# Kernel tuning notes

Measured on AMD Instinct MI355X. Metric: run time of the kernel, lower is better.

Reference implementation:

```python
import jax, jax.numpy as jnp
from jax import lax
import numpy as np

ALPHA = 0.5; EPS = 1e-6; RANK_PAIRS = 100
W_MEAN = 0.5; W_STD = 0.5
L_STAT = 1.0; L_RANK = 1.0; L_SMOOTH = 1.0
LABELS = np.array([5, 8, 13], dtype=np.int32)
TGT_CV = np.array([0.077, 0.227, 0.348], dtype=np.float32)


def _erode(mask_f):
    # torch: 1 - max_pool2d(1-x, k=3, pad=1); implicit -inf padding means
    # out-of-bounds pixels act as foreground -> min-pool with +inf init.
    return lax.reduce_window(mask_f, jnp.inf, lax.min, (3, 3), (1, 1), 'SAME') > 0.5


def _per_region(pred, pix, region, tgt_cv, key):
    # pred, pix: [H,W] float; region: [H,W] bool
    H, W = pred.shape
    HW = H * W
    regf = region.astype(jnp.float32)
    e1 = _erode(regf)
    e2 = _erode(e1.astype(jnp.float32))  # erode(region, iterations=2)
    core1 = jnp.where(jnp.sum(e1) < 2, region, e1)
    core2 = jnp.where(jnp.sum(e2) < 3, core1, e2)
    n_reg = jnp.sum(region)

    # ---- std (coefficient-of-variation) term on core2
    c2 = core2.astype(jnp.float32)
    n2 = jnp.sum(c2)
    n2s = jnp.maximum(n2, 1.0)
    mu = jnp.sum(pred * c2) / n2s
    var = jnp.sum(c2 * (pred - mu) ** 2) / n2s  # unbiased=False
    cv = jnp.sqrt(var) / (jnp.abs(mu) + EPS)
    std_val = jnp.abs(cv - tgt_cv)
    std_valid = (n_reg >= 3) & (n2 >= 3)

    # ---- pairwise rank term on core1 (sampled-pair path; realistic regions
    # always have n > full_pair_threshold=20)
    c1f = core1.reshape(-1).astype(jnp.float32)
    n1 = jnp.sum(c1f)
    p = jnp.where(n1 > 0, c1f / jnp.maximum(n1, 1.0), 1.0 / HW)
    k1, k2 = jax.random.split(key)
    ii = jax.random.choice(k1, HW, (RANK_PAIRS,), replace=True, p=p)
    jj = jax.random.choice(k2, HW, (RANK_PAIRS,), replace=True, p=p)
    pf = pred.reshape(-1)
    xf = pix.reshape(-1)
    s = jnp.sign(xf[ii] - xf[jj])
    pv = ((ii != jj) & (s != 0)).astype(jnp.float32)
    hinge = jax.nn.relu(-(pf[ii] - pf[jj]) * s)
    npv = jnp.sum(pv)
    rank_val = jnp.sum(hinge * pv) / jnp.maximum(npv, 1.0)
    rank_valid = (n_reg >= 2) & (n1 >= 2) & (npv > 0)

    # ---- smoothness term on core2
    dx = jnp.abs(pred[:, 1:] - pred[:, :-1])
    mx = (core2[:, 1:] & core2[:, :-1]).astype(jnp.float32)
    dy = jnp.abs(pred[1:, :] - pred[:-1, :])
    my = (core2[1:, :] & core2[:-1, :]).astype(jnp.float32)
    cx = jnp.sum(mx); cy = jnp.sum(my)
    mean_x = jnp.sum(dx * mx) / jnp.maximum(cx, 1.0)
    mean_y = jnp.sum(dy * my) / jnp.maximum(cy, 1.0)
    hx = (cx > 0).astype(jnp.float32); hy = (cy > 0).astype(jnp.float32)
    npres = hx + hy
    smooth_val = (mean_x * hx + mean_y * hy) / jnp.maximum(npres, 1.0)
    smooth_valid = (n_reg >= 3) & (n2 >= 3) & (npres > 0)

    return std_val, std_valid, rank_val, rank_valid, smooth_val, smooth_valid


def _masked_mean(v, valid):
    vf = valid.astype(jnp.float32)
    c = jnp.sum(vf)
    return jnp.where(c > 0, jnp.sum(v * vf) / jnp.maximum(c, 1.0), 0.0)


def _forward(pred, target, lab14, img1, img2):
    B, _, H, W = pred.shape
    p2 = pred[:, 0]
    lab = lab14[:, 0]
    t1 = img1[:, 0]
    t2 = img2[:, 0]
    pix = (1.0 - ALPHA) * (1.0 - t1) + ALPHA * t2  # pixel_map
    loss_mean = jnp.mean(jnp.abs(pred - target))

    labels = jnp.asarray(LABELS)
    regions = lab[:, None, :, :] == labels[None, :, None, None]  # [B,3,H,W]
    R = regions.reshape(B * 3, H, W)
    P = jnp.broadcast_to(p2[:, None], (B, 3, H, W)).reshape(B * 3, H, W)
    X = jnp.broadcast_to(pix[:, None], (B, 3, H, W)).reshape(B * 3, H, W)
    T = jnp.tile(jnp.asarray(TGT_CV), B)  # [B*3], label-minor matches reshape
    keys = jax.random.split(jax.random.key(42), B * 3)

    sv, svd, rv, rvd, mv, mvd = jax.vmap(_per_region)(P, X, R, T, keys)
    loss_std = _masked_mean(sv, svd)
    loss_rank = _masked_mean(rv, rvd)
    loss_smooth = _masked_mean(mv, mvd)

    loss_stat = W_MEAN * loss_mean + W_STD * loss_std
    return L_STAT * loss_stat + L_RANK * loss_rank + L_SMOOTH * loss_smooth


def setup_inputs() -> dict:
    key = jax.random.key(0)
    k1, k2, k3, k4, k5 = jax.random.split(key, 5)
    B, H, W = 16, 512, 512
    pred = jax.random.normal(k1, (B, 1, H, W), dtype=jnp.float32)
    target = jax.random.normal(k2, (B, 1, H, W), dtype=jnp.float32)
    lab14 = jax.random.randint(k3, (B, 1, H, W), 0, 15, dtype=jnp.int32)
    img1 = jax.random.uniform(k4, (B, 1, H, W), dtype=jnp.float32)
    img2 = jax.random.uniform(k5, (B, 1, H, W), dtype=jnp.float32)
    return {"pred": pred, "target": target, "lab14": lab14, "img1": img1, "img2": img2}


def reference(pred, target, lab14, img1, img2):
    return _forward(pred, target, lab14, img1, img2)
```

## Files before the change

kernel.cpp:

```cpp
#include <hip/hip_runtime.h>

#define BB 16
#define HH 512
#define WW 512
#define BH 8
#define NR (BH+5)
#define NBANDS (HH/BH)
#define NBLK (NBANDS*BB)
#define NREG 48
#define HWTOT (HH*WW)
#define MASK13 0x1FFFu

#define OFF_CNT48  0
#define OFF_SUM48  2048
#define OFF_RANKV  4608
#define OFF_RANKD  4800
#define OFF_CTR    5120
#define OFF_SUMSP  8192
#define OFF_CNTP   (OFF_SUMSP + NBLK*40*4)
#define OFF_MREG   (OFF_CNTP + NBLK*28*4)
#define MASKBYTES  (48LL*512*8*8)
#define OFF_ME1    (OFF_MREG + MASKBYTES)

__device__ __forceinline__ unsigned int hashu(unsigned int x) {
  x ^= x >> 16; x *= 0x7feb352dU; x ^= x >> 15; x *= 0x846ca68bU; x ^= x >> 16;
  return x;
}

__global__ __launch_bounds__(512, 4) void pass1_kernel(
    const float* __restrict__ pred, const float* __restrict__ target,
    const int* __restrict__ lab,
    float* __restrict__ sumsP, int* __restrict__ countsP,
    unsigned long long* __restrict__ mRegG, unsigned long long* __restrict__ mE1G,
    int* __restrict__ ctr)
{
  __shared__ unsigned long long XCH[514];
  __shared__ unsigned long long NB0[512];
  __shared__ unsigned int      NB2[512];
  __shared__ float RED[8][37];
  __shared__ unsigned int CNT[8][14];

  const int t    = threadIdx.x;
  const int lane = t & 63;
  const int wv   = t >> 6;
  const int c    = t;
  const int r0   = blockIdx.x * BH;
  const int b    = blockIdx.y;
  const int R    = r0 - 3;
  const int bandblk = b * NBANDS + blockIdx.x;

  if (blockIdx.x == 0 && b == 0 && t == 0) *ctr = 0;

  unsigned int OOR = 0;
  {
    int topClip = -R;
    if (topClip > 0) OOR |= (1u << topClip) - 1u;
    int botStart = HH - R;
    if (botStart < NR) OOR |= (~0u << botStart) & ((1u << NR) - 1u);
  }

  unsigned int colm0 = 0, colm1 = 0, colm2 = 0;
  #pragma unroll
  for (int lr = 0; lr < NR; ++lr) {
    int gy = R + lr;
    if ((unsigned)gy < (unsigned)HH) {
      int l = lab[((size_t)b*HH + gy)*WW + c];
      colm0 |= (l == 5)  ? (1u << lr) : 0u;
      colm1 |= (l == 8)  ? (1u << lr) : 0u;
      colm2 |= (l == 13) ? (1u << lr) : 0u;
    }
  }

  unsigned long long pk =  (unsigned long long)(colm0 | OOR)
        | ((unsigned long long)(colm1 | OOR) << 13)
        | ((unsigned long long)(colm2 | OOR) << 26);
  XCH[c+1] = pk;
  if (t == 0) { XCH[0] = ~0ull; XCH[513] = ~0ull; }
  __syncthreads();
  unsigned long long hp = pk & XCH[c] & XCH[c+2];
  unsigned int e1a[3];
  #pragma unroll
  for (int li = 0; li < 3; ++li) {
    unsigned int h = (unsigned int)((hp >> (13*li)) & MASK13);
    e1a[li] = h & (h >> 1) & (h << 1);
  }
  __syncthreads();
  unsigned long long pk2 =  (unsigned long long)((e1a[0] | OOR) & MASK13)
        | ((unsigned long long)((e1a[1] | OOR) & MASK13) << 13)
        | ((unsigned long long)((e1a[2] | OOR) & MASK13) << 26);
  XCH[c+1] = pk2;
  __syncthreads();
  unsigned long long hp2 = pk2 & XCH[c] & XCH[c+2];
  unsigned int e2a[3];
  #pragma unroll
  for (int li = 0; li < 3; ++li) {
    unsigned int h = (unsigned int)((hp2 >> (13*li)) & MASK13);
    e2a[li] = h & (h >> 1) & (h << 1);
  }

  unsigned int mS[9] = { colm0, e1a[0], e2a[0],
                         colm1, e1a[1], e2a[1],
                         colm2, e1a[2], e2a[2] };

  {
    unsigned long long p0 = 0;
    #pragma unroll
    for (int cb = 0; cb < 8; ++cb) p0 |= (unsigned long long)((mS[cb] >> 3) & 0xFFu) << (cb*8);
    NB0[c] = p0; NB2[c] = (mS[8] >> 3) & 0xFFu;
  }
  __syncthreads();
  unsigned long long nb0 = (c < 511) ? NB0[c+1] : 0ull;
  unsigned int       nb2 = (c < 511) ? NB2[c+1] : 0u;

  unsigned int W[9];
  const unsigned int nOOR = ~OOR;
  #pragma unroll
  for (int cb = 0; cb < 9; ++cb) {
    unsigned int w8  = (mS[cb] >> 3) & 0xFFu;
    unsigned int nbw = (cb < 8) ? ((unsigned int)(nb0 >> (cb*8)) & 0xFFu) : (nb2 & 0xFFu);
    unsigned int px8 = w8 & nbw;
    unsigned int mcl = mS[cb] & nOOR;
    unsigned int py8 = ((mcl & (mcl << 1)) >> 3) & 0xFFu;
    W[cb] = w8 | (px8 << 8) | (py8 << 16);
  }

  {
    unsigned long long myWord = 0;
    #pragma unroll
    for (int k = 0; k < 48; ++k) {
      const int ktype = k / 24, krem = k % 24, kli = krem >> 3, krow = krem & 7;
      unsigned int bit = (W[kli*3 + ktype] >> krow) & 1u;
      unsigned long long wrd = __ballot(bit != 0u);
      if (lane == k) myWord = wrd;
    }
    if (lane < 48) {
      int type = lane / 24, rem = lane % 24, li = rem >> 3, row = rem & 7;
      int gy = r0 + row;
      unsigned long long* dst = type ? mE1G : mRegG;
      dst[(((size_t)(b*3 + li))*HH + gy)*8 + wv] = myWord;
    }
  }

  {
    unsigned int pkc[14];
    #pragma unroll
    for (int j = 0; j < 14; ++j) pkc[j] = 0;
    #pragma unroll
    for (int cb = 0; cb < 9; ++cb) {
      unsigned int cnt = __popc(W[cb] & 0x0000FFu);
      unsigned int cx  = __popc(W[cb] & 0x00FF00u);
      unsigned int cy  = __popc(W[cb] & 0xFF0000u);
      int k0 = cb*3;
      pkc[(k0  )>>1] |= cnt << (((k0  )&1)*16);
      pkc[(k0+1)>>1] |= cx  << (((k0+1)&1)*16);
      pkc[(k0+2)>>1] |= cy  << (((k0+2)&1)*16);
    }
    #pragma unroll
    for (int j = 0; j < 14; ++j) {
      unsigned int v = pkc[j];
      for (int off = 32; off; off >>= 1) v += __shfl_down(v, off);
      if (lane == 0) CNT[wv][j] = v;
    }
  }

  float aP[9] = {}, aP2[9] = {}, aDX[9] = {}, aDY[9] = {};
  float aAbs = 0.f;
  const float* pB = pred   + (size_t)b*HH*WW;
  const float* tB = target + (size_t)b*HH*WW;
  float p_prev = (r0 > 0) ? pB[(size_t)(r0-1)*WW + c] : 0.f;
  const int cR = (c < 511) ? c + 1 : c;

  #pragma unroll
  for (int row = 0; row < BH; ++row) {
    const int gy = r0 + row;
    const float* prow = pB + (size_t)gy*WW;
    float p  = prow[c];
    float pr = prow[cR];
    float tg = tB[(size_t)gy*WW + c];
    aAbs += fabsf(p - tg);
    float d = fabsf(pr - p);
    float v = fabsf(p - p_prev);
    #pragma unroll
    for (int cb = 0; cb < 9; ++cb) {
      unsigned int c1 = (W[cb] >> row) & 1u;
      unsigned int px = (W[cb] >> (row + 8)) & 1u;
      unsigned int py = (W[cb] >> (row + 16)) & 1u;
      float f = c1 ? p : 0.f;
      aP[cb]  += f;
      aP2[cb]  = fmaf(f, p, aP2[cb]);
      aDX[cb] += px ? d : 0.f;
      aDY[cb] += py ? v : 0.f;
    }
    p_prev = p;
  }

  #pragma unroll
  for (int cb = 0; cb < 9; ++cb) {
    float s0 = aP[cb], s1 = aP2[cb], s2 = aDX[cb], s3 = aDY[cb];
    for (int off = 32; off; off >>= 1) {
      s0 += __shfl_down(s0, off);
      s1 += __shfl_down(s1, off);
      s2 += __shfl_down(s2, off);
      s3 += __shfl_down(s3, off);
    }
    if (lane == 0) {
      RED[wv][0*9 + cb] = s0; RED[wv][1*9 + cb] = s1;
      RED[wv][2*9 + cb] = s2; RED[wv][3*9 + cb] = s3;
    }
  }
  {
    float va = aAbs;
    for (int off = 32; off; off >>= 1) va += __shfl_down(va, off);
    if (lane == 0) RED[wv][36] = va;
  }
  __syncthreads();

  if (t < 37) {
    float s = 0.f;
    #pragma unroll
    for (int w = 0; w < 8; ++w) s += RED[w][t];
    sumsP[(size_t)bandblk*40 + t] = s;
  }
  if (t < 14) {
    unsigned int s = 0;
    #pragma unroll
    for (int w = 0; w < 8; ++w) s += CNT[w][t];
    countsP[bandblk*28 + 2*t]     = (int)(s & 0xFFFFu);
    countsP[bandblk*28 + 2*t + 1] = (int)(s >> 16);
  }
}

__global__ __launch_bounds__(256) void pass2_kernel(
    const float* __restrict__ pred, const float* __restrict__ img1,
    const float* __restrict__ img2,
    const unsigned long long* __restrict__ mRegG,
    const unsigned long long* __restrict__ mE1G,
    const float* __restrict__ sumsP, const int* __restrict__ countsP,
    int* __restrict__ counts48, float* __restrict__ sums48,
    float* __restrict__ rankval, int* __restrict__ rankvalid,
    int* __restrict__ ctr, float* __restrict__ out)
{
  const int r = blockIdx.x;
  const int b = r / 3, li = r % 3;
  const int t = threadIdx.x;
  const int lane = t & 63;
  const int wv   = t >> 6;
  __shared__ int LC[9];
  __shared__ int rowc[HH];
  __shared__ int pre[HH];
  __shared__ int grpPre[64];
  __shared__ int idxArr[200];
  __shared__ float redH[4];
  __shared__ int   redP[4];
  __shared__ int lastFlag;
  __shared__ double svvS[NREG], smvS[NREG];
  __shared__ int svdS[NREG], smdS[NREG];
  __shared__ double SAB[4];

  if (t < 9) LC[t] = 0;
  __syncthreads();
  for (int k = t; k < 9*NBANDS; k += 256) {
    int s9 = k >> 6, band = k & 63;
    int m = s9 / 3, st = s9 % 3;
    atomicAdd(&LC[s9], countsP[(b*NBANDS + band)*28 + (li*3 + m)*3 + st]);
  }
  if (wv == 0) {
    float sp[12];
    #pragma unroll
    for (int j = 0; j < 12; ++j) {
      int stat = j / 3, m = j % 3;
      sp[j] = sumsP[(size_t)(b*NBANDS + lane)*40 + stat*9 + li*3 + m];
    }
    #pragma unroll
    for (int j = 0; j < 12; ++j)
      for (int off = 32; off; off >>= 1) sp[j] += __shfl_down(sp[j], off);
    if (lane == 0) {
      #pragma unroll
      for (int j = 0; j < 12; ++j) atomicExch(&sums48[r*12 + j], sp[j]);
    }
  }
  __syncthreads();
  if (t < 9) atomicExch(&counts48[r*9 + t], LC[t]);

  int n_reg = LC[0], n_e1 = LC[3];
  int useE1 = (n_e1 >= 2);
  int n1 = useE1 ? n_e1 : n_reg;
  bool doRank = (n_reg >= 2 && n1 >= 2);
  float rv = 0.f; int rvd = 0;

  if (doRank) {
    const unsigned long long* M = (useE1 ? mE1G : mRegG) + (size_t)r*HH*8;
    {
      int row = t*2;
      int c0 = 0, c1v = 0;
      #pragma unroll
      for (int w = 0; w < 8; ++w) c0 += __popcll(M[(size_t)row*8 + w]);
      #pragma unroll
      for (int w = 0; w < 8; ++w) c1v += __popcll(M[(size_t)(row+1)*8 + w]);
      rowc[row] = c0; rowc[row+1] = c1v;
    }
    __syncthreads();
    if (t < 64) {
      int base = t*8, s = 0;
      #pragma unroll
      for (int k = 0; k < 8; ++k) s += rowc[base + k];
      int v = s;
      for (int off = 1; off < 64; off <<= 1) {
        int o = __shfl_up(v, off);
        if (t >= off) v += o;
      }
      grpPre[t] = v - s;
    }
    __syncthreads();
    if (t < 64) {
      int s = grpPre[t], base = t*8;
      #pragma unroll
      for (int k = 0; k < 8; ++k) { pre[base + k] = s; s += rowc[base + k]; }
    }
    __syncthreads();

    if (t < 200) {
      unsigned int h = hashu(0x9e3779b9u + (unsigned)(r*200 + t));
      float u = (float)(h >> 8) * (1.0f / 16777216.0f);
      int k = (int)(u * (float)n1);
      if (k >= n1) k = n1 - 1;
      if (k < 0) k = 0;
      int lo = 0, hi = HH;
      while (hi - lo > 1) { int mid = (lo + hi) >> 1; if (pre[mid] <= k) lo = mid; else hi = mid; }
      int row = lo;
      int local = k - pre[row];
      int idx = 0;
      #pragma unroll
      for (int w = 0; w < 8; ++w) {
        unsigned long long mm = M[(size_t)row*8 + w];
        int cc = __popcll(mm);
        if (local < cc) {
          for (int i = 0; i < local; ++i) mm &= mm - 1;
          idx = row*WW + w*64 + __builtin_ctzll(mm);
          local = 1 << 20;
        } else {
          local -= cc;
        }
      }
      idxArr[t] = idx;
    }
    __syncthreads();

    float hv = 0.f; int pv = 0;
    if (t < 100) {
      int ii = idxArr[t], jj = idxArr[t+100];
      size_t base = (size_t)b * HWTOT;
      float pi = pred[base+ii], pj = pred[base+jj];
      float xi = 0.5f*(1.f - img1[base+ii]) + 0.5f*img2[base+ii];
      float xj = 0.5f*(1.f - img1[base+jj]) + 0.5f*img2[base+jj];
      float s = (xi > xj) ? 1.f : ((xi < xj) ? -1.f : 0.f);
      pv = (ii != jj) && (s != 0.f);
      float hinge = fmaxf(0.f, -(pi - pj)*s);
      hv = pv ? hinge : 0.f;
    }
    for (int off = 32; off; off >>= 1) {
      hv += __shfl_down(hv, off);
      pv += __shfl_down(pv, off);
    }
    if (lane == 0) { redH[wv] = hv; redP[wv] = pv; }
    __syncthreads();
    if (t == 0) {
      float sh = redH[0] + redH[1] + redH[2] + redH[3];
      int   sp = redP[0] + redP[1] + redP[2] + redP[3];
      rv  = sh / (float)(sp > 0 ? sp : 1);
      rvd = (sp > 0) ? 1 : 0;
    }
  }

  __syncthreads();
  if (t == 0) {
    atomicExch(&rankval[r], rv);
    atomicExch(&rankvalid[r], rvd);
    __threadfence();
    int old = atomicAdd(ctr, 1);
    lastFlag = (old == NREG - 1);
  }
  __syncthreads();

  if (lastFlag) {
    __threadfence();
    double pa = 0.0;
    for (int k = t; k < NBLK; k += 256) pa += (double)sumsP[(size_t)k*40 + 36];
    for (int off = 32; off; off >>= 1) pa += __shfl_down(pa, off);
    if (lane == 0) SAB[wv] = pa;
    if (t < NREG) {
      const int* C = counts48 + t*9;
      const float* S = sums48 + t*12;
      int nr = C[0], ne1 = C[3], ne2 = C[6];
      int m1 = (ne1 < 2) ? 0 : 1;
      int m2 = (ne2 < 3) ? m1 : 2;
      int n2 = C[m2*3];
      double n2s = (double)(n2 > 1 ? n2 : 1);
      double mu  = (double)S[m2] / n2s;
      double var = (double)S[3+m2] / n2s - mu*mu;
      if (var < 0.0) var = 0.0;
      double cv = sqrt(var) / (fabs(mu) + 1e-6);
      int tli = t % 3;
      double tcv = (tli == 0) ? 0.077 : ((tli == 1) ? 0.227 : 0.348);
      svvS[t] = fabs(cv - tcv);
      svdS[t] = (nr >= 3 && n2 >= 3);
      int cx = C[m2*3+1], cy = C[m2*3+2];
      double mean_x = (double)S[6+m2] / (double)(cx > 1 ? cx : 1);
      double mean_y = (double)S[9+m2] / (double)(cy > 1 ? cy : 1);
      int hx = (cx > 0), hy = (cy > 0);
      int npres = hx + hy;
      smvS[t] = (mean_x*hx + mean_y*hy) / (double)(npres > 1 ? npres : 1);
      smdS[t] = (nr >= 3 && n2 >= 3 && npres > 0);
    }
    __syncthreads();
    if (t == 0) {
      double s_std = 0, s_sm = 0, s_rk = 0;
      int c_std = 0, c_sm = 0, c_rk = 0;
      for (int i = 0; i < NREG; ++i) {
        if (svdS[i])       { s_std += svvS[i];     c_std++; }
        if (smdS[i])       { s_sm  += smvS[i];     c_sm++;  }
        if (rankvalid[i])  { s_rk  += rankval[i];  c_rk++;  }
      }
      double loss_std = c_std ? s_std / c_std : 0.0;
      double loss_sm  = c_sm  ? s_sm  / c_sm  : 0.0;
      double loss_rk  = c_rk  ? s_rk  / c_rk  : 0.0;
      double loss_mean = (SAB[0] + SAB[1] + SAB[2] + SAB[3])
                         / (double)((long long)BB * HWTOT);
      out[0] = (float)(0.5*loss_mean + 0.5*loss_std + loss_rk + loss_sm);
    }
  }
}

extern "C" void kernel_launch(void* const* d_in, const int* in_sizes, int n_in,
                              void* d_out, int out_size, void* d_ws, size_t ws_size,
                              hipStream_t stream) {
  const float* pred   = (const float*)d_in[0];
  const float* target = (const float*)d_in[1];
  const int*   lab    = (const int*)d_in[2];
  const float* img1   = (const float*)d_in[3];
  const float* img2   = (const float*)d_in[4];
  float* out = (float*)d_out;
  char* ws = (char*)d_ws;

  int*    counts48 = (int*)(ws + OFF_CNT48);
  float*  sums48   = (float*)(ws + OFF_SUM48);
  float*  rankval  = (float*)(ws + OFF_RANKV);
  int*    rankvld  = (int*)(ws + OFF_RANKD);
  int*    ctr      = (int*)(ws + OFF_CTR);
  float*  sumsP    = (float*)(ws + OFF_SUMSP);
  int*    countsP  = (int*)(ws + OFF_CNTP);
  unsigned long long* mReg = (unsigned long long*)(ws + OFF_MREG);
  unsigned long long* mE1  = (unsigned long long*)(ws + OFF_ME1);

  dim3 g1(NBANDS, BB);
  pass1_kernel<<<g1, 512, 0, stream>>>(pred, target, lab, sumsP, countsP,
                                       mReg, mE1, ctr);
  pass2_kernel<<<NREG, 256, 0, stream>>>(pred, img1, img2, mReg, mE1,
                                         sumsP, countsP, counts48, sums48,
                                         rankval, rankvld, ctr, out);
}
```

Baseline: 167.7 us.

## Double pass1 band height and precompute per-row mask popcounts for pass2

```diff
diff --git a/kernel.cpp b/kernel.cpp
--- a/kernel.cpp
+++ b/kernel.cpp
@@ -3,13 +3,13 @@
 #define BB 16
 #define HH 512
 #define WW 512
-#define BH 8
+#define BH 16
 #define NR (BH+5)
 #define NBANDS (HH/BH)
 #define NBLK (NBANDS*BB)
 #define NREG 48
 #define HWTOT (HH*WW)
-#define MASK13 0x1FFFu
+#define MASK21 0x1FFFFFu
 
 #define OFF_CNT48  0
 #define OFF_SUM48  2048
@@ -18,7 +18,9 @@
 #define OFF_CTR    5120
 #define OFF_SUMSP  8192
 #define OFF_CNTP   (OFF_SUMSP + NBLK*40*4)
-#define OFF_MREG   (OFF_CNTP + NBLK*28*4)
+#define OFF_ROWCR  (OFF_CNTP + NBLK*28*4)
+#define OFF_ROWCE  (OFF_ROWCR + 48*512*4)
+#define OFF_MREG   (OFF_ROWCE + 48*512*4)
 #define MASKBYTES  (48LL*512*8*8)
 #define OFF_ME1    (OFF_MREG + MASKBYTES)
 
@@ -32,11 +34,14 @@
     const int* __restrict__ lab,
     float* __restrict__ sumsP, int* __restrict__ countsP,
     unsigned long long* __restrict__ mRegG, unsigned long long* __restrict__ mE1G,
+    int* __restrict__ rowcR, int* __restrict__ rowcE,
     int* __restrict__ ctr)
 {
   __shared__ unsigned long long XCH[514];
   __shared__ unsigned long long NB0[512];
+  __shared__ unsigned long long NB1[512];
   __shared__ unsigned int      NB2[512];
+  __shared__ int   RC[96];
   __shared__ float RED[8][37];
   __shared__ unsigned int CNT[8][14];
 
@@ -50,6 +55,7 @@
   const int bandblk = b * NBANDS + blockIdx.x;
 
   if (blockIdx.x == 0 && b == 0 && t == 0) *ctr = 0;
+  if (t < 96) RC[t] = 0;
 
   unsigned int OOR = 0;
   {
@@ -60,7 +66,6 @@
   }
 
   unsigned int colm0 = 0, colm1 = 0, colm2 = 0;
-  #pragma unroll
   for (int lr = 0; lr < NR; ++lr) {
     int gy = R + lr;
     if ((unsigned)gy < (unsigned)HH) {
@@ -72,8 +77,8 @@
   }
 
   unsigned long long pk =  (unsigned long long)(colm0 | OOR)
-        | ((unsigned long long)(colm1 | OOR) << 13)
-        | ((unsigned long long)(colm2 | OOR) << 26);
+        | ((unsigned long long)(colm1 | OOR) << 21)
+        | ((unsigned long long)(colm2 | OOR) << 42);
   XCH[c+1] = pk;
   if (t == 0) { XCH[0] = ~0ull; XCH[513] = ~0ull; }
   __syncthreads();
@@ -81,20 +86,20 @@
   unsigned int e1a[3];
   #pragma unroll
   for (int li = 0; li < 3; ++li) {
-    unsigned int h = (unsigned int)((hp >> (13*li)) & MASK13);
+    unsigned int h = (unsigned int)((hp >> (21*li)) & MASK21);
     e1a[li] = h & (h >> 1) & (h << 1);
   }
   __syncthreads();
-  unsigned long long pk2 =  (unsigned long long)((e1a[0] | OOR) & MASK13)
-        | ((unsigned long long)((e1a[1] | OOR) & MASK13) << 13)
-        | ((unsigned long long)((e1a[2] | OOR) & MASK13) << 26);
+  unsigned long long pk2 =  (unsigned long long)((e1a[0] | OOR) & MASK21)
+        | ((unsigned long long)((e1a[1] | OOR) & MASK21) << 21)
+        | ((unsigned long long)((e1a[2] | OOR) & MASK21) << 42);
   XCH[c+1] = pk2;
   __syncthreads();
   unsigned long long hp2 = pk2 & XCH[c] & XCH[c+2];
   unsigned int e2a[3];
   #pragma unroll
   for (int li = 0; li < 3; ++li) {
-    unsigned int h = (unsigned int)((hp2 >> (13*li)) & MASK13);
+    unsigned int h = (unsigned int)((hp2 >> (21*li)) & MASK21);
     e2a[li] = h & (h >> 1) & (h << 1);
   }
 
@@ -103,41 +108,55 @@
                          colm2, e1a[2], e2a[2] };
 
   {
-    unsigned long long p0 = 0;
-    #pragma unroll
-    for (int cb = 0; cb < 8; ++cb) p0 |= (unsigned long long)((mS[cb] >> 3) & 0xFFu) << (cb*8);
-    NB0[c] = p0; NB2[c] = (mS[8] >> 3) & 0xFFu;
+    unsigned long long p0 = 0, p1 = 0;
+    #pragma unroll
+    for (int cb = 0; cb < 4; ++cb) p0 |= (unsigned long long)((mS[cb] >> 3) & 0xFFFFu) << (cb*16);
+    #pragma unroll
+    for (int cb = 4; cb < 8; ++cb) p1 |= (unsigned long long)((mS[cb] >> 3) & 0xFFFFu) << ((cb-4)*16);
+    NB0[c] = p0; NB1[c] = p1; NB2[c] = (mS[8] >> 3) & 0xFFFFu;
   }
   __syncthreads();
   unsigned long long nb0 = (c < 511) ? NB0[c+1] : 0ull;
+  unsigned long long nb1 = (c < 511) ? NB1[c+1] : 0ull;
   unsigned int       nb2 = (c < 511) ? NB2[c+1] : 0u;
 
-  unsigned int W[9];
+  unsigned int W[9], Y[9];
   const unsigned int nOOR = ~OOR;
   #pragma unroll
   for (int cb = 0; cb < 9; ++cb) {
-    unsigned int w8  = (mS[cb] >> 3) & 0xFFu;
-    unsigned int nbw = (cb < 8) ? ((unsigned int)(nb0 >> (cb*8)) & 0xFFu) : (nb2 & 0xFFu);
-    unsigned int px8 = w8 & nbw;
+    unsigned int w16 = (mS[cb] >> 3) & 0xFFFFu;
+    unsigned int nbw;
+    if (cb < 4)      nbw = (unsigned int)(nb0 >> (cb*16)) & 0xFFFFu;
+    else if (cb < 8) nbw = (unsigned int)(nb1 >> ((cb-4)*16)) & 0xFFFFu;
+    else             nbw = nb2 & 0xFFFFu;
     unsigned int mcl = mS[cb] & nOOR;
-    unsigned int py8 = ((mcl & (mcl << 1)) >> 3) & 0xFFu;
-    W[cb] = w8 | (px8 << 8) | (py8 << 16);
-  }
-
-  {
-    unsigned long long myWord = 0;
-    #pragma unroll
-    for (int k = 0; k < 48; ++k) {
-      const int ktype = k / 24, krem = k % 24, kli = krem >> 3, krow = krem & 7;
+    unsigned int py16 = ((mcl & (mcl << 1)) >> 3) & 0xFFFFu;
+    W[cb] = w16 | ((w16 & nbw) << 16);
+    Y[cb] = py16;
+  }
+
+  {
+    unsigned long long w1 = 0, w2 = 0;
+    #pragma unroll
+    for (int k = 0; k < 96; ++k) {
+      const int ktype = k / 48, krem = k % 48, kli = krem >> 4, krow = krem & 15;
       unsigned int bit = (W[kli*3 + ktype] >> krow) & 1u;
       unsigned long long wrd = __ballot(bit != 0u);
-      if (lane == k) myWord = wrd;
-    }
-    if (lane < 48) {
-      int type = lane / 24, rem = lane % 24, li = rem >> 3, row = rem & 7;
-      int gy = r0 + row;
+      if (k < 64) { if (lane == k) w1 = wrd; }
+      else        { if (lane == (k-64)) w2 = wrd; }
+    }
+    {
+      int k = lane;
+      int type = k / 48, rem = k % 48, li = rem >> 4, row = rem & 15;
       unsigned long long* dst = type ? mE1G : mRegG;
-      dst[(((size_t)(b*3 + li))*HH + gy)*8 + wv] = myWord;
+      dst[(((size_t)(b*3 + li))*HH + (r0 + row))*8 + wv] = w1;
+      atomicAdd(&RC[k], (int)__popcll(w1));
+    }
+    if (lane < 32) {
+      int k = 64 + lane;
+      int rem = k % 48, li = rem >> 4, row = rem & 15;
+      mE1G[(((size_t)(b*3 + li))*HH + (r0 + row))*8 + wv] = w2;
+      atomicAdd(&RC[k], (int)__popcll(w2));
     }
   }
 
@@ -147,9 +166,9 @@
     for (int j = 0; j < 14; ++j) pkc[j] = 0;
     #pragma unroll
     for (int cb = 0; cb < 9; ++cb) {
-      unsigned int cnt = __popc(W[cb] & 0x0000FFu);
-      unsigned int cx  = __popc(W[cb] & 0x00FF00u);
-      unsigned int cy  = __popc(W[cb] & 0xFF0000u);
+      unsigned int cnt = __popc(W[cb] & 0xFFFFu);
+      unsigned int cx  = __popc(W[cb] >> 16);
+      unsigned int cy  = __popc(Y[cb]);
       int k0 = cb*3;
       pkc[(k0  )>>1] |= cnt << (((k0  )&1)*16);
       pkc[(k0+1)>>1] |= cx  << (((k0+1)&1)*16);
@@ -170,7 +189,6 @@
   float p_prev = (r0 > 0) ? pB[(size_t)(r0-1)*WW + c] : 0.f;
   const int cR = (c < 511) ? c + 1 : c;
 
-  #pragma unroll
   for (int row = 0; row < BH; ++row) {
     const int gy = r0 + row;
     const float* prow = pB + (size_t)gy*WW;
@@ -183,8 +201,8 @@
     #pragma unroll
     for (int cb = 0; cb < 9; ++cb) {
       unsigned int c1 = (W[cb] >> row) & 1u;
-      unsigned int px = (W[cb] >> (row + 8)) & 1u;
-      unsigned int py = (W[cb] >> (row + 16)) & 1u;
+      unsigned int px = (W[cb] >> (row + 16)) & 1u;
+      unsigned int py = (Y[cb] >> row) & 1u;
       float f = c1 ? p : 0.f;
       aP[cb]  += f;
       aP2[cb]  = fmaf(f, p, aP2[cb]);
@@ -228,6 +246,11 @@
     countsP[bandblk*28 + 2*t]     = (int)(s & 0xFFFFu);
     countsP[bandblk*28 + 2*t + 1] = (int)(s >> 16);
   }
+  if (t < 96) {
+    int type = t / 48, rem = t % 48, li = rem >> 4, row = rem & 15;
+    int* dst = type ? rowcE : rowcR;
+    dst[((size_t)(b*3 + li))*HH + (r0 + row)] = RC[t];
+  }
 }
 
 __global__ __launch_bounds__(256) void pass2_kernel(
@@ -236,6 +259,7 @@
     const unsigned long long* __restrict__ mRegG,
     const unsigned long long* __restrict__ mE1G,
     const float* __restrict__ sumsP, const int* __restrict__ countsP,
+    const int* __restrict__ rowcR, const int* __restrict__ rowcE,
     int* __restrict__ counts48, float* __restrict__ sums48,
     float* __restrict__ rankval, int* __restrict__ rankvalid,
     int* __restrict__ ctr, float* __restrict__ out)
@@ -246,9 +270,10 @@
   const int lane = t & 63;
   const int wv   = t >> 6;
   __shared__ int LC[9];
-  __shared__ int rowc[HH];
+  __shared__ int rcR[HH], rcE[HH];
   __shared__ int pre[HH];
   __shared__ int grpPre[64];
+  __shared__ int wsumR[4], wsumE[4];
   __shared__ int idxArr[200];
   __shared__ float redH[4];
   __shared__ int   redP[4];
@@ -258,18 +283,34 @@
   __shared__ double SAB[4];
 
   if (t < 9) LC[t] = 0;
-  __syncthreads();
+
+  int2 vR = ((const int2*)(rowcR + (size_t)r*HH))[t];
+  int2 vE = ((const int2*)(rowcE + (size_t)r*HH))[t];
+  rcR[2*t] = vR.x; rcR[2*t+1] = vR.y;
+  rcE[2*t] = vE.x; rcE[2*t+1] = vE.y;
+  {
+    int sR = vR.x + vR.y, sE = vE.x + vE.y;
+    for (int off = 32; off; off >>= 1) {
+      sR += __shfl_down(sR, off);
+      sE += __shfl_down(sE, off);
+    }
+    if (lane == 0) { wsumR[wv] = sR; wsumE[wv] = sE; }
+  }
+  __syncthreads();
+  int n_reg = wsumR[0] + wsumR[1] + wsumR[2] + wsumR[3];
+  int n_e1  = wsumE[0] + wsumE[1] + wsumE[2] + wsumE[3];
+
   for (int k = t; k < 9*NBANDS; k += 256) {
-    int s9 = k >> 6, band = k & 63;
-    int m = s9 / 3, st = s9 % 3;
-    atomicAdd(&LC[s9], countsP[(b*NBANDS + band)*28 + (li*3 + m)*3 + st]);
+    int s9 = k >> 5, band = k & 31;
+    atomicAdd(&LC[s9], countsP[(b*NBANDS + band)*28 + (li*3 + (s9/3))*3 + (s9%3)]);
   }
   if (wv == 0) {
     float sp[12];
     #pragma unroll
     for (int j = 0; j < 12; ++j) {
       int stat = j / 3, m = j % 3;
-      sp[j] = sumsP[(size_t)(b*NBANDS + lane)*40 + stat*9 + li*3 + m];
+      sp[j] = (lane < NBANDS)
+            ? sumsP[(size_t)(b*NBANDS + lane)*40 + stat*9 + li*3 + m] : 0.f;
     }
     #pragma unroll
     for (int j = 0; j < 12; ++j)
@@ -282,28 +323,17 @@
   __syncthreads();
   if (t < 9) atomicExch(&counts48[r*9 + t], LC[t]);
 
-  int n_reg = LC[0], n_e1 = LC[3];
   int useE1 = (n_e1 >= 2);
   int n1 = useE1 ? n_e1 : n_reg;
   bool doRank = (n_reg >= 2 && n1 >= 2);
   float rv = 0.f; int rvd = 0;
 
   if (doRank) {
-    const unsigned long long* M = (useE1 ? mE1G : mRegG) + (size_t)r*HH*8;
-    {
-      int row = t*2;
-      int c0 = 0, c1v = 0;
-      #pragma unroll
-      for (int w = 0; w < 8; ++w) c0 += __popcll(M[(size_t)row*8 + w]);
-      #pragma unroll
-      for (int w = 0; w < 8; ++w) c1v += __popcll(M[(size_t)(row+1)*8 + w]);
-      rowc[row] = c0; rowc[row+1] = c1v;
-    }
-    __syncthreads();
+    const int* rc = useE1 ? rcE : rcR;
     if (t < 64) {
       int base = t*8, s = 0;
       #pragma unroll
-      for (int k = 0; k < 8; ++k) s += rowc[base + k];
+      for (int k = 0; k < 8; ++k) s += rc[base + k];
       int v = s;
       for (int off = 1; off < 64; off <<= 1) {
         int o = __shfl_up(v, off);
@@ -315,10 +345,11 @@
     if (t < 64) {
       int s = grpPre[t], base = t*8;
       #pragma unroll
-      for (int k = 0; k < 8; ++k) { pre[base + k] = s; s += rowc[base + k]; }
+      for (int k = 0; k < 8; ++k) { pre[base + k] = s; s += rc[base + k]; }
     }
     __syncthreads();
 
+    const unsigned long long* M = (useE1 ? mE1G : mRegG) + (size_t)r*HH*8;
     if (t < 200) {
       unsigned int h = hashu(0x9e3779b9u + (unsigned)(r*200 + t));
       float u = (float)(h >> 8) * (1.0f / 16777216.0f);
@@ -449,13 +480,16 @@
   int*    ctr      = (int*)(ws + OFF_CTR);
   float*  sumsP    = (float*)(ws + OFF_SUMSP);
   int*    countsP  = (int*)(ws + OFF_CNTP);
+  int*    rowcR    = (int*)(ws + OFF_ROWCR);
+  int*    rowcE    = (int*)(ws + OFF_ROWCE);
   unsigned long long* mReg = (unsigned long long*)(ws + OFF_MREG);
   unsigned long long* mE1  = (unsigned long long*)(ws + OFF_ME1);
 
   dim3 g1(NBANDS, BB);
   pass1_kernel<<<g1, 512, 0, stream>>>(pred, target, lab, sumsP, countsP,
-                                       mReg, mE1, ctr);
+                                       mReg, mE1, rowcR, rowcE, ctr);
   pass2_kernel<<<NREG, 256, 0, stream>>>(pred, img1, img2, mReg, mE1,
-                                         sumsP, countsP, counts48, sums48,
+                                         sumsP, countsP, rowcR, rowcE,
+                                         counts48, sums48,
                                          rankval, rankvld, ctr, out);
 }
```

Measured after the change: 169.0 us. Within noise of the previous version (+0.8%).

## Accumulate stats only for core2 masks and compute fallbacks lazily in pass2

Applied to the files above, without the earlier changes.

```diff
diff --git a/kernel.cpp b/kernel.cpp
--- a/kernel.cpp
+++ b/kernel.cpp
@@ -11,16 +11,20 @@
 #define HWTOT (HH*WW)
 #define MASK13 0x1FFFu
 
-#define OFF_CNT48  0
-#define OFF_SUM48  2048
-#define OFF_RANKV  4608
-#define OFF_RANKD  4800
-#define OFF_CTR    5120
-#define OFF_SUMSP  8192
-#define OFF_CNTP   (OFF_SUMSP + NBLK*40*4)
-#define OFF_MREG   (OFF_CNTP + NBLK*28*4)
-#define MASKBYTES  (48LL*512*8*8)
-#define OFF_ME1    (OFF_MREG + MASKBYTES)
+#define OFF_SVV   0
+#define OFF_SVD   192
+#define OFF_SMV   384
+#define OFF_SMD   576
+#define OFF_RANKV 768
+#define OFF_RANKD 960
+#define OFF_CTR   1152
+#define OFF_SUMSP 4096
+#define OFF_CNTP  (OFF_SUMSP + NBLK*16*4)
+#define OFF_ROWCR (OFF_CNTP + NBLK*16*4)
+#define OFF_ROWCE (OFF_ROWCR + 48*512*4)
+#define OFF_MREG  (OFF_ROWCE + 48*512*4)
+#define MASKBYTES (48LL*512*8*8)
+#define OFF_ME1   (OFF_MREG + MASKBYTES)
 
 __device__ __forceinline__ unsigned int hashu(unsigned int x) {
   x ^= x >> 16; x *= 0x7feb352dU; x ^= x >> 15; x *= 0x846ca68bU; x ^= x >> 16;
@@ -32,13 +36,14 @@
     const int* __restrict__ lab,
     float* __restrict__ sumsP, int* __restrict__ countsP,
     unsigned long long* __restrict__ mRegG, unsigned long long* __restrict__ mE1G,
+    int* __restrict__ rowcR, int* __restrict__ rowcE,
     int* __restrict__ ctr)
 {
   __shared__ unsigned long long XCH[514];
-  __shared__ unsigned long long NB0[512];
-  __shared__ unsigned int      NB2[512];
-  __shared__ float RED[8][37];
-  __shared__ unsigned int CNT[8][14];
+  __shared__ unsigned int NBX[512];
+  __shared__ int   RC[48];
+  __shared__ float RED[8][13];
+  __shared__ unsigned int CNT[8][8];
 
   const int t    = threadIdx.x;
   const int lane = t & 63;
@@ -47,9 +52,10 @@
   const int r0   = blockIdx.x * BH;
   const int b    = blockIdx.y;
   const int R    = r0 - 3;
-  const int bandblk = b * NBANDS + blockIdx.x;
+  const int blk  = b * NBANDS + blockIdx.x;
 
   if (blockIdx.x == 0 && b == 0 && t == 0) *ctr = 0;
+  if (t < 48) RC[t] = 0;
 
   unsigned int OOR = 0;
   {
@@ -102,68 +108,62 @@
                          colm1, e1a[1], e2a[1],
                          colm2, e1a[2], e2a[2] };
 
-  {
-    unsigned long long p0 = 0;
-    #pragma unroll
-    for (int cb = 0; cb < 8; ++cb) p0 |= (unsigned long long)((mS[cb] >> 3) & 0xFFu) << (cb*8);
-    NB0[c] = p0; NB2[c] = (mS[8] >> 3) & 0xFFu;
-  }
-  __syncthreads();
-  unsigned long long nb0 = (c < 511) ? NB0[c+1] : 0ull;
-  unsigned int       nb2 = (c < 511) ? NB2[c+1] : 0u;
-
-  unsigned int W[9];
+  NBX[c] =  ((e2a[0] >> 3) & 0xFFu)
+         | (((e2a[1] >> 3) & 0xFFu) << 8)
+         | (((e2a[2] >> 3) & 0xFFu) << 16);
+  __syncthreads();
+  unsigned int nbx = (c < 511) ? NBX[c+1] : 0u;
+
+  unsigned int W2[3];
   const unsigned int nOOR = ~OOR;
   #pragma unroll
-  for (int cb = 0; cb < 9; ++cb) {
-    unsigned int w8  = (mS[cb] >> 3) & 0xFFu;
-    unsigned int nbw = (cb < 8) ? ((unsigned int)(nb0 >> (cb*8)) & 0xFFu) : (nb2 & 0xFFu);
-    unsigned int px8 = w8 & nbw;
-    unsigned int mcl = mS[cb] & nOOR;
+  for (int li = 0; li < 3; ++li) {
+    unsigned int w8  = (e2a[li] >> 3) & 0xFFu;
+    unsigned int nbw = (nbx >> (8*li)) & 0xFFu;
+    unsigned int mcl = e2a[li] & nOOR;
     unsigned int py8 = ((mcl & (mcl << 1)) >> 3) & 0xFFu;
-    W[cb] = w8 | (px8 << 8) | (py8 << 16);
+    W2[li] = w8 | ((w8 & nbw) << 8) | (py8 << 16);
   }
 
   {
-    unsigned long long myWord = 0;
+    unsigned long long w1 = 0;
     #pragma unroll
     for (int k = 0; k < 48; ++k) {
       const int ktype = k / 24, krem = k % 24, kli = krem >> 3, krow = krem & 7;
-      unsigned int bit = (W[kli*3 + ktype] >> krow) & 1u;
+      unsigned int bit = (mS[kli*3 + ktype] >> (krow + 3)) & 1u;
       unsigned long long wrd = __ballot(bit != 0u);
-      if (lane == k) myWord = wrd;
+      if (lane == k) w1 = wrd;
     }
     if (lane < 48) {
       int type = lane / 24, rem = lane % 24, li = rem >> 3, row = rem & 7;
-      int gy = r0 + row;
       unsigned long long* dst = type ? mE1G : mRegG;
-      dst[(((size_t)(b*3 + li))*HH + gy)*8 + wv] = myWord;
+      dst[(((size_t)(b*3 + li))*HH + (r0 + row))*8 + wv] = w1;
+      atomicAdd(&RC[lane], (int)__popcll(w1));
     }
   }
 
   {
-    unsigned int pkc[14];
-    #pragma unroll
-    for (int j = 0; j < 14; ++j) pkc[j] = 0;
-    #pragma unroll
-    for (int cb = 0; cb < 9; ++cb) {
-      unsigned int cnt = __popc(W[cb] & 0x0000FFu);
-      unsigned int cx  = __popc(W[cb] & 0x00FF00u);
-      unsigned int cy  = __popc(W[cb] & 0xFF0000u);
-      int k0 = cb*3;
-      pkc[(k0  )>>1] |= cnt << (((k0  )&1)*16);
-      pkc[(k0+1)>>1] |= cx  << (((k0+1)&1)*16);
-      pkc[(k0+2)>>1] |= cy  << (((k0+2)&1)*16);
-    }
-    #pragma unroll
-    for (int j = 0; j < 14; ++j) {
+    unsigned int v15[15];
+    #pragma unroll
+    for (int cb = 0; cb < 9; ++cb) v15[cb] = __popc((mS[cb] >> 3) & 0xFFu);
+    #pragma unroll
+    for (int li = 0; li < 3; ++li) {
+      v15[9+li]  = __popc(W2[li] & 0x00FF00u);
+      v15[12+li] = __popc(W2[li] & 0xFF0000u);
+    }
+    unsigned int pkc[8];
+    #pragma unroll
+    for (int j = 0; j < 7; ++j) pkc[j] = v15[2*j] | (v15[2*j+1] << 16);
+    pkc[7] = v15[14];
+    #pragma unroll
+    for (int j = 0; j < 8; ++j) {
       unsigned int v = pkc[j];
       for (int off = 32; off; off >>= 1) v += __shfl_down(v, off);
       if (lane == 0) CNT[wv][j] = v;
     }
   }
 
-  float aP[9] = {}, aP2[9] = {}, aDX[9] = {}, aDY[9] = {};
+  float aP[3] = {}, aP2[3] = {}, aDX[3] = {}, aDY[3] = {};
   float aAbs = 0.f;
   const float* pB = pred   + (size_t)b*HH*WW;
   const float* tB = target + (size_t)b*HH*WW;
@@ -181,52 +181,49 @@
     float d = fabsf(pr - p);
     float v = fabsf(p - p_prev);
     #pragma unroll
-    for (int cb = 0; cb < 9; ++cb) {
-      unsigned int c1 = (W[cb] >> row) & 1u;
-      unsigned int px = (W[cb] >> (row + 8)) & 1u;
-      unsigned int py = (W[cb] >> (row + 16)) & 1u;
+    for (int li = 0; li < 3; ++li) {
+      unsigned int c1 = (W2[li] >> row) & 1u;
+      unsigned int px = (W2[li] >> (row + 8)) & 1u;
+      unsigned int py = (W2[li] >> (row + 16)) & 1u;
       float f = c1 ? p : 0.f;
-      aP[cb]  += f;
-      aP2[cb]  = fmaf(f, p, aP2[cb]);
-      aDX[cb] += px ? d : 0.f;
-      aDY[cb] += py ? v : 0.f;
+      aP[li]  += f;
+      aP2[li]  = fmaf(f, p, aP2[li]);
+      aDX[li] += px ? d : 0.f;
+      aDY[li] += py ? v : 0.f;
     }
     p_prev = p;
   }
 
-  #pragma unroll
-  for (int cb = 0; cb < 9; ++cb) {
-    float s0 = aP[cb], s1 = aP2[cb], s2 = aDX[cb], s3 = aDY[cb];
-    for (int off = 32; off; off >>= 1) {
-      s0 += __shfl_down(s0, off);
-      s1 += __shfl_down(s1, off);
-      s2 += __shfl_down(s2, off);
-      s3 += __shfl_down(s3, off);
-    }
-    if (lane == 0) {
-      RED[wv][0*9 + cb] = s0; RED[wv][1*9 + cb] = s1;
-      RED[wv][2*9 + cb] = s2; RED[wv][3*9 + cb] = s3;
-    }
-  }
   {
-    float va = aAbs;
-    for (int off = 32; off; off >>= 1) va += __shfl_down(va, off);
-    if (lane == 0) RED[wv][36] = va;
-  }
-  __syncthreads();
-
-  if (t < 37) {
+    float a13[13] = { aP[0], aP2[0], aDX[0], aDY[0],
+                      aP[1], aP2[1], aDX[1], aDY[1],
+                      aP[2], aP2[2], aDX[2], aDY[2], aAbs };
+    #pragma unroll
+    for (int j = 0; j < 13; ++j) {
+      float s = a13[j];
+      for (int off = 32; off; off >>= 1) s += __shfl_down(s, off);
+      if (lane == 0) RED[wv][j] = s;
+    }
+  }
+  __syncthreads();
+
+  if (t < 13) {
     float s = 0.f;
     #pragma unroll
     for (int w = 0; w < 8; ++w) s += RED[w][t];
-    sumsP[(size_t)bandblk*40 + t] = s;
-  }
-  if (t < 14) {
+    sumsP[(size_t)blk*16 + t] = s;
+  }
+  if (t < 8) {
     unsigned int s = 0;
     #pragma unroll
     for (int w = 0; w < 8; ++w) s += CNT[w][t];
-    countsP[bandblk*28 + 2*t]     = (int)(s & 0xFFFFu);
-    countsP[bandblk*28 + 2*t + 1] = (int)(s >> 16);
+    countsP[blk*16 + 2*t] = (int)(s & 0xFFFFu);
+    if (2*t + 1 < 15) countsP[blk*16 + 2*t + 1] = (int)(s >> 16);
+  }
+  if (t < 48) {
+    int type = t / 24, rem = t % 24, li = rem >> 3, row = rem & 7;
+    int* dst = type ? rowcE : rowcR;
+    dst[((size_t)(b*3 + li))*HH + (r0 + row)] = RC[t];
   }
 }
 
@@ -236,8 +233,10 @@
     const unsigned long long* __restrict__ mRegG,
     const unsigned long long* __restrict__ mE1G,
     const float* __restrict__ sumsP, const int* __restrict__ countsP,
-    int* __restrict__ counts48, float* __restrict__ sums48,
-    float* __restrict__ rankval, int* __restrict__ rankvalid,
+    const int* __restrict__ rowcR, const int* __restrict__ rowcE,
+    float* __restrict__ svvG, int* __restrict__ svdG,
+    float* __restrict__ smvG, int* __restrict__ smdG,
+    float* __restrict__ rankvG, int* __restrict__ rankdG,
     int* __restrict__ ctr, float* __restrict__ out)
 {
   const int r = blockIdx.x;
@@ -245,65 +244,109 @@
   const int t = threadIdx.x;
   const int lane = t & 63;
   const int wv   = t >> 6;
-  __shared__ int LC[9];
-  __shared__ int rowc[HH];
+  __shared__ int rcR[HH], rcE[HH];
   __shared__ int pre[HH];
   __shared__ int grpPre[64];
+  __shared__ int LC[5];
+  __shared__ float SP[4];
+  __shared__ float FBf[4][4];
+  __shared__ int   FBi[4][2];
   __shared__ int idxArr[200];
   __shared__ float redH[4];
   __shared__ int   redP[4];
   __shared__ int lastFlag;
   __shared__ double svvS[NREG], smvS[NREG];
   __shared__ int svdS[NREG], smdS[NREG];
+  __shared__ float rkvS[NREG];
+  __shared__ int   rkdS[NREG];
   __shared__ double SAB[4];
 
-  if (t < 9) LC[t] = 0;
-  __syncthreads();
-  for (int k = t; k < 9*NBANDS; k += 256) {
-    int s9 = k >> 6, band = k & 63;
-    int m = s9 / 3, st = s9 % 3;
-    atomicAdd(&LC[s9], countsP[(b*NBANDS + band)*28 + (li*3 + m)*3 + st]);
+  if (t < 5) LC[t] = 0;
+  int2 vR = ((const int2*)(rowcR + (size_t)r*HH))[t];
+  int2 vE = ((const int2*)(rowcE + (size_t)r*HH))[t];
+  rcR[2*t] = vR.x; rcR[2*t+1] = vR.y;
+  rcE[2*t] = vE.x; rcE[2*t+1] = vE.y;
+  __syncthreads();
+
+  for (int k = t; k < 5*NBANDS; k += 256) {
+    int s5 = k >> 6, band = k & 63;
+    int j = (s5 < 3) ? (li*3 + s5) : ((s5 == 3) ? (9 + li) : (12 + li));
+    atomicAdd(&LC[s5], countsP[(b*NBANDS + band)*16 + j]);
   }
   if (wv == 0) {
-    float sp[12];
-    #pragma unroll
-    for (int j = 0; j < 12; ++j) {
-      int stat = j / 3, m = j % 3;
-      sp[j] = sumsP[(size_t)(b*NBANDS + lane)*40 + stat*9 + li*3 + m];
-    }
-    #pragma unroll
-    for (int j = 0; j < 12; ++j)
-      for (int off = 32; off; off >>= 1) sp[j] += __shfl_down(sp[j], off);
+    float sp[4];
+    #pragma unroll
+    for (int s = 0; s < 4; ++s)
+      sp[s] = sumsP[(size_t)(b*NBANDS + lane)*16 + li*4 + s];
+    #pragma unroll
+    for (int s = 0; s < 4; ++s)
+      for (int off = 32; off; off >>= 1) sp[s] += __shfl_down(sp[s], off);
+    if (lane == 0) { SP[0]=sp[0]; SP[1]=sp[1]; SP[2]=sp[2]; SP[3]=sp[3]; }
+  }
+  __syncthreads();
+
+  const int n_reg = LC[0], n_e1 = LC[1], n_e2 = LC[2];
+  const int m1 = (n_e1 < 2) ? 0 : 1;
+  const int m2 = (n_e2 < 3) ? m1 : 2;
+
+  float fP = 0.f, fP2 = 0.f, fDX = 0.f, fDY = 0.f;
+  int fCX = 0, fCY = 0;
+  if (m2 != 2) {
+    const unsigned long long* M2 = ((m2 == 1) ? mE1G : mRegG) + (size_t)r*HH*8;
+    const float* pB = pred + (size_t)b*HWTOT;
+    #pragma unroll
+    for (int rr = 0; rr < 2; ++rr) {
+      int row = t + rr*256;
+      const unsigned long long* mrow = M2 + (size_t)row*8;
+      const float* prow = pB + (size_t)row*WW;
+      for (int w = 0; w < 8; ++w) {
+        unsigned long long mm = mrow[w];
+        unsigned long long cc = mm;
+        while (cc) {
+          int i = __builtin_ctzll(cc); cc &= cc - 1;
+          float p = prow[w*64 + i];
+          fP += p; fP2 = fmaf(p, p, fP2);
+        }
+        unsigned long long nxt = (w < 7) ? mrow[w+1] : 0ull;
+        unsigned long long pm = mm & ((mm >> 1) | (nxt << 63));
+        while (pm) {
+          int i = __builtin_ctzll(pm); pm &= pm - 1;
+          fDX += fabsf(prow[w*64 + i + 1] - prow[w*64 + i]); fCX++;
+        }
+        if (row > 0) {
+          unsigned long long qm = mm & mrow[w - 8];
+          while (qm) {
+            int i = __builtin_ctzll(qm); qm &= qm - 1;
+            fDY += fabsf(prow[w*64 + i] - prow[w*64 + i - WW]); fCY++;
+          }
+        }
+      }
+    }
+  }
+  {
+    float s0=fP, s1=fP2, s2=fDX, s3=fDY; int i0=fCX, i1=fCY;
+    for (int off = 32; off; off >>= 1) {
+      s0 += __shfl_down(s0, off); s1 += __shfl_down(s1, off);
+      s2 += __shfl_down(s2, off); s3 += __shfl_down(s3, off);
+      i0 += __shfl_down(i0, off); i1 += __shfl_down(i1, off);
+    }
     if (lane == 0) {
-      #pragma unroll
-      for (int j = 0; j < 12; ++j) atomicExch(&sums48[r*12 + j], sp[j]);
-    }
-  }
-  __syncthreads();
-  if (t < 9) atomicExch(&counts48[r*9 + t], LC[t]);
-
-  int n_reg = LC[0], n_e1 = LC[3];
+      FBf[wv][0]=s0; FBf[wv][1]=s1; FBf[wv][2]=s2; FBf[wv][3]=s3;
+      FBi[wv][0]=i0; FBi[wv][1]=i1;
+    }
+  }
+
   int useE1 = (n_e1 >= 2);
   int n1 = useE1 ? n_e1 : n_reg;
   bool doRank = (n_reg >= 2 && n1 >= 2);
   float rv = 0.f; int rvd = 0;
 
   if (doRank) {
-    const unsigned long long* M = (useE1 ? mE1G : mRegG) + (size_t)r*HH*8;
-    {
-      int row = t*2;
-      int c0 = 0, c1v = 0;
-      #pragma unroll
-      for (int w = 0; w < 8; ++w) c0 += __popcll(M[(size_t)row*8 + w]);
-      #pragma unroll
-      for (int w = 0; w < 8; ++w) c1v += __popcll(M[(size_t)(row+1)*8 + w]);
-      rowc[row] = c0; rowc[row+1] = c1v;
-    }
-    __syncthreads();
+    const int* rc = useE1 ? rcE : rcR;
     if (t < 64) {
       int base = t*8, s = 0;
       #pragma unroll
-      for (int k = 0; k < 8; ++k) s += rowc[base + k];
+      for (int k = 0; k < 8; ++k) s += rc[base + k];
       int v = s;
       for (int off = 1; off < 64; off <<= 1) {
         int o = __shfl_up(v, off);
@@ -315,10 +358,11 @@
     if (t < 64) {
       int s = grpPre[t], base = t*8;
       #pragma unroll
-      for (int k = 0; k < 8; ++k) { pre[base + k] = s; s += rowc[base + k]; }
+      for (int k = 0; k < 8; ++k) { pre[base + k] = s; s += rc[base + k]; }
     }
     __syncthreads();
 
+    const unsigned long long* M = (useE1 ? mE1G : mRegG) + (size_t)r*HH*8;
     if (t < 200) {
       unsigned int h = hashu(0x9e3779b9u + (unsigned)(r*200 + t));
       float u = (float)(h >> 8) * (1.0f / 16777216.0f);
@@ -363,19 +407,45 @@
       pv += __shfl_down(pv, off);
     }
     if (lane == 0) { redH[wv] = hv; redP[wv] = pv; }
-    __syncthreads();
-    if (t == 0) {
+  }
+  __syncthreads();
+
+  if (t == 0) {
+    if (doRank) {
       float sh = redH[0] + redH[1] + redH[2] + redH[3];
       int   sp = redP[0] + redP[1] + redP[2] + redP[3];
       rv  = sh / (float)(sp > 0 ? sp : 1);
       rvd = (sp > 0) ? 1 : 0;
     }
-  }
-
-  __syncthreads();
-  if (t == 0) {
-    atomicExch(&rankval[r], rv);
-    atomicExch(&rankvalid[r], rvd);
+    double S0, S1, S2, S3; int n2, cx, cy;
+    if (m2 == 2) {
+      S0 = SP[0]; S1 = SP[1]; S2 = SP[2]; S3 = SP[3];
+      n2 = n_e2; cx = LC[3]; cy = LC[4];
+    } else {
+      S0 = (double)(FBf[0][0]+FBf[1][0]+FBf[2][0]+FBf[3][0]);
+      S1 = (double)(FBf[0][1]+FBf[1][1]+FBf[2][1]+FBf[3][1]);
+      S2 = (double)(FBf[0][2]+FBf[1][2]+FBf[2][2]+FBf[3][2]);
+      S3 = (double)(FBf[0][3]+FBf[1][3]+FBf[2][3]+FBf[3][3]);
+      n2 = (m2 == 1) ? n_e1 : n_reg;
+      cx = FBi[0][0]+FBi[1][0]+FBi[2][0]+FBi[3][0];
+      cy = FBi[0][1]+FBi[1][1]+FBi[2][1]+FBi[3][1];
+    }
+    double n2s = (double)(n2 > 1 ? n2 : 1);
+    double mu  = S0 / n2s;
+    double var = S1 / n2s - mu*mu;
+    if (var < 0.0) var = 0.0;
+    double cv = sqrt(var) / (fabs(mu) + 1e-6);
+    double tcv = (li == 0) ? 0.077 : ((li == 1) ? 0.227 : 0.348);
+    double mean_x = S2 / (double)(cx > 1 ? cx : 1);
+    double mean_y = S3 / (double)(cy > 1 ? cy : 1);
+    int hx = (cx > 0), hy = (cy > 0);
+    int npres = hx + hy;
+    atomicExch(&svvG[r], (float)fabs(cv - tcv));
+    atomicExch(&svdG[r], (int)(n_reg >= 3 && n2 >= 3));
+    atomicExch(&smvG[r], (float)((mean_x*hx + mean_y*hy) / (double)(npres > 1 ? npres : 1)));
+    atomicExch(&smdG[r], (int)(n_reg >= 3 && n2 >= 3 && npres > 0));
+    atomicExch(&rankvG[r], rv);
+    atomicExch(&rankdG[r], rvd);
     __threadfence();
     int old = atomicAdd(ctr, 1);
     lastFlag = (old == NREG - 1);
@@ -385,41 +455,22 @@
   if (lastFlag) {
     __threadfence();
     double pa = 0.0;
-    for (int k = t; k < NBLK; k += 256) pa += (double)sumsP[(size_t)k*40 + 36];
+    for (int k = t; k < NBLK; k += 256) pa += (double)sumsP[(size_t)k*16 + 12];
     for (int off = 32; off; off >>= 1) pa += __shfl_down(pa, off);
     if (lane == 0) SAB[wv] = pa;
     if (t < NREG) {
-      const int* C = counts48 + t*9;
-      const float* S = sums48 + t*12;
-      int nr = C[0], ne1 = C[3], ne2 = C[6];
-      int m1 = (ne1 < 2) ? 0 : 1;
-      int m2 = (ne2 < 3) ? m1 : 2;
-      int n2 = C[m2*3];
-      double n2s = (double)(n2 > 1 ? n2 : 1);
-      double mu  = (double)S[m2] / n2s;
-      double var = (double)S[3+m2] / n2s - mu*mu;
-      if (var < 0.0) var = 0.0;
-      double cv = sqrt(var) / (fabs(mu) + 1e-6);
-      int tli = t % 3;
-      double tcv = (tli == 0) ? 0.077 : ((tli == 1) ? 0.227 : 0.348);
-      svvS[t] = fabs(cv - tcv);
-      svdS[t] = (nr >= 3 && n2 >= 3);
-      int cx = C[m2*3+1], cy = C[m2*3+2];
-      double mean_x = (double)S[6+m2] / (double)(cx > 1 ? cx : 1);
-      double mean_y = (double)S[9+m2] / (double)(cy > 1 ? cy : 1);
-      int hx = (cx > 0), hy = (cy > 0);
-      int npres = hx + hy;
-      smvS[t] = (mean_x*hx + mean_y*hy) / (double)(npres > 1 ? npres : 1);
-      smdS[t] = (nr >= 3 && n2 >= 3 && npres > 0);
+      svvS[t] = (double)svvG[t]; svdS[t] = svdG[t];
+      smvS[t] = (double)smvG[t]; smdS[t] = smdG[t];
+      rkvS[t] = rankvG[t];       rkdS[t] = rankdG[t];
     }
     __syncthreads();
     if (t == 0) {
       double s_std = 0, s_sm = 0, s_rk = 0;
       int c_std = 0, c_sm = 0, c_rk = 0;
       for (int i = 0; i < NREG; ++i) {
-        if (svdS[i])       { s_std += svvS[i];     c_std++; }
-        if (smdS[i])       { s_sm  += smvS[i];     c_sm++;  }
-        if (rankvalid[i])  { s_rk  += rankval[i];  c_rk++;  }
+        if (svdS[i]) { s_std += svvS[i]; c_std++; }
+        if (smdS[i]) { s_sm  += smvS[i]; c_sm++;  }
+        if (rkdS[i]) { s_rk  += (double)rkvS[i]; c_rk++; }
       }
       double loss_std = c_std ? s_std / c_std : 0.0;
       double loss_sm  = c_sm  ? s_sm  / c_sm  : 0.0;
@@ -442,20 +493,25 @@
   float* out = (float*)d_out;
   char* ws = (char*)d_ws;
 
-  int*    counts48 = (int*)(ws + OFF_CNT48);
-  float*  sums48   = (float*)(ws + OFF_SUM48);
-  float*  rankval  = (float*)(ws + OFF_RANKV);
-  int*    rankvld  = (int*)(ws + OFF_RANKD);
-  int*    ctr      = (int*)(ws + OFF_CTR);
-  float*  sumsP    = (float*)(ws + OFF_SUMSP);
-  int*    countsP  = (int*)(ws + OFF_CNTP);
+  float* svvG   = (float*)(ws + OFF_SVV);
+  int*   svdG   = (int*)(ws + OFF_SVD);
+  float* smvG   = (float*)(ws + OFF_SMV);
+  int*   smdG   = (int*)(ws + OFF_SMD);
+  float* rankvG = (float*)(ws + OFF_RANKV);
+  int*   rankdG = (int*)(ws + OFF_RANKD);
+  int*   ctr    = (int*)(ws + OFF_CTR);
+  float* sumsP  = (float*)(ws + OFF_SUMSP);
+  int*   countsP= (int*)(ws + OFF_CNTP);
+  int*   rowcR  = (int*)(ws + OFF_ROWCR);
+  int*   rowcE  = (int*)(ws + OFF_ROWCE);
   unsigned long long* mReg = (unsigned long long*)(ws + OFF_MREG);
   unsigned long long* mE1  = (unsigned long long*)(ws + OFF_ME1);
 
   dim3 g1(NBANDS, BB);
   pass1_kernel<<<g1, 512, 0, stream>>>(pred, target, lab, sumsP, countsP,
-                                       mReg, mE1, ctr);
+                                       mReg, mE1, rowcR, rowcE, ctr);
   pass2_kernel<<<NREG, 256, 0, stream>>>(pred, img1, img2, mReg, mE1,
-                                         sumsP, countsP, counts48, sums48,
-                                         rankval, rankvld, ctr, out);
+                                         sumsP, countsP, rowcR, rowcE,
+                                         svvG, svdG, smvG, smdG,
+                                         rankvG, rankdG, ctr, out);
 }
```

Result: slower. 217.8 us (+29.9%).
